# Performance work log

Measured on AMD Instinct MI355X. Metric: run time of the kernel, lower is better.

## Reference

```python
import jax
import jax.numpy as jnp
from jax import lax
import numpy as np

ALPHA_RISE = 0.5
ALPHA_FALL = 0.99


def setup_inputs() -> dict:
    key = jax.random.key(0)
    x = jax.random.normal(key, (16, 4096, 1024), dtype=jnp.float32)
    return {"x": x}


def reference(x):
    # x: [B, T, C]; asymmetric EMA scanned over T with data-dependent alpha.
    B, T, C = x.shape
    dt = x.dtype

    def step(carry, xt):
        y_prev, not_first = carry  # [B,C], [B,1]
        falling = (y_prev - xt > 0).astype(dt)  # Gt0: 1.0 if falling else 0.0
        alpha = falling * ALPHA_FALL + (1.0 - falling) * ALPHA_RISE
        y_upd = alpha * y_prev + (1.0 - alpha) * xt
        y = not_first * y_upd + (1.0 - not_first) * xt  # first frame passes x through
        return (y, jnp.ones_like(not_first)), y

    y0 = jnp.zeros((B, C), dt)
    nf0 = jnp.zeros((B, 1), dt)
    _, ys = lax.scan(step, (y0, nf0), jnp.swapaxes(x, 0, 1))  # ys: [T,B,C]
    return jnp.swapaxes(ys, 0, 1)
```

## Files before the change

### kernel.cpp

```cpp
#include <hip/hip_runtime.h>


constexpr int B = 16;
constexpr int T = 4096;
constexpr int C = 1024;
constexpr int U = 32;
constexpr int NSEQ = B * C;
constexpr int NCHUNK = 8;
constexpr int CHUNK = T / NCHUNK;
constexpr int WARM = 640;

__device__ inline float ema_step(float y, float xv) {
  const float d = y - xv;
  return fmaxf(__builtin_fmaf(0.99f, d, xv), __builtin_fmaf(0.5f, d, xv));
}

template <bool STORE>
__device__ inline void run_steps(const float* __restrict__ xp,
                                 float* __restrict__ op, float& y,
                                 int t_from, int t_to) {
  const int n = t_to - t_from;
  const int ngrp = n / U;
  const float* p = xp + (size_t)t_from * (size_t)C;
  float* q = op + (size_t)t_from * (size_t)C;

  float b0[U], b1[U];
  auto load = [&](float* buf, int g) {
    const float* pp = p + (size_t)g * (size_t)U * (size_t)C;
#pragma unroll
    for (int j = 0; j < U; ++j) buf[j] = pp[(size_t)j * (size_t)C];
  };
  auto comp = [&](const float* buf, int g) {
    float* qq = q + (size_t)g * (size_t)U * (size_t)C;
#pragma unroll
    for (int j = 0; j < U; ++j) {
      y = ema_step(y, buf[j]);
      if (STORE) qq[(size_t)j * (size_t)C] = y;
    }
  };

  if (ngrp >= 1) load(b0, 0);
  if (ngrp >= 2) load(b1, 1);
  int g = 0;
  while (g < ngrp) {
    comp(b0, g);
    if (g + 2 < ngrp) load(b0, g + 2);
    ++g;
    if (g >= ngrp) break;
    comp(b1, g);
    if (g + 2 < ngrp) load(b1, g + 2);
    ++g;
  }

  const int r = n - ngrp * U;
  if (r > 0) {
    float br[U];
    const float* pp = p + (size_t)ngrp * (size_t)U * (size_t)C;
    float* qq = q + (size_t)ngrp * (size_t)U * (size_t)C;
#pragma unroll
    for (int j = 0; j < U; ++j)
      if (j < r) br[j] = pp[(size_t)j * (size_t)C];
#pragma unroll
    for (int j = 0; j < U; ++j)
      if (j < r) {
        y = ema_step(y, br[j]);
        if (STORE) qq[(size_t)j * (size_t)C] = y;
      }
  }
}

__global__ __launch_bounds__(64) void AsymmetricEMA_kernel(
    const float* __restrict__ x, float* __restrict__ out) {
  const int tid = blockIdx.x * 64 + threadIdx.x;
  const int b = tid >> 10;
  const int c = tid & (C - 1);
  const size_t base = (size_t)b * (size_t)T * (size_t)C + (size_t)c;
  const float* __restrict__ xp = x + base;
  float* __restrict__ op = out + base;

  const int chunk = blockIdx.y;
  const int t_lo = chunk * CHUNK;
  const int t_hi = t_lo + CHUNK;

  if (chunk == 0) {
    float y = xp[0];
    op[0] = y;
    run_steps<true>(xp, op, y, 1, t_hi);
  } else {
    int s0 = t_lo - WARM;
    if (s0 < 0) s0 = 0;
    float y = xp[(size_t)s0 * (size_t)C];
    run_steps<false>(xp, op, y, s0 + 1, t_lo);
    run_steps<true>(xp, op, y, t_lo, t_hi);
  }
}

extern "C" void kernel_launch(void* const* d_in, const int* in_sizes, int n_in,
                              void* d_out, int out_size, void* d_ws, size_t ws_size,
                              hipStream_t stream) {
  const float* x = (const float*)d_in[0];
  float* out = (float*)d_out;
  dim3 grid(NSEQ / 64, NCHUNK);
  AsymmetricEMA_kernel<<<grid, 64, 0, stream>>>(x, out);
}
```

Baseline: 476.7 us.

## Vectorize EMA scan to float4 per thread and double time chunks

Each thread now handles four adjacent channels through float4 loads and stores, giving 128-bit memory transactions and fewer per-element address computations. To keep enough threads in flight with a quarter as many lanes, the time axis is split into 16 chunks instead of 8, and the unroll depth drops to 16 to limit register pressure. The extra chunks add more warm-up recomputation (WARM steps per chunk), which raises redundant read traffic. The warm-up also remains an approximation that depends on the EMA decay to converge.

```diff
diff --git a/kernel.cpp b/kernel.cpp
--- a/kernel.cpp
+++ b/kernel.cpp
@@ -4,38 +4,49 @@
 constexpr int B = 16;
 constexpr int T = 4096;
 constexpr int C = 1024;
-constexpr int U = 32;
-constexpr int NSEQ = B * C;
-constexpr int NCHUNK = 8;
+constexpr int VEC = 4;
+constexpr int CV = C / VEC;
+constexpr int U = 16;
+constexpr int NTHREADS = B * CV;
+constexpr int NCHUNK = 16;
 constexpr int CHUNK = T / NCHUNK;
 constexpr int WARM = 640;
 
-__device__ inline float ema_step(float y, float xv) {
+__device__ inline float ema1(float y, float xv) {
   const float d = y - xv;
   return fmaxf(__builtin_fmaf(0.99f, d, xv), __builtin_fmaf(0.5f, d, xv));
 }
 
+__device__ inline float4 ema4(float4 y, float4 xv) {
+  float4 r;
+  r.x = ema1(y.x, xv.x);
+  r.y = ema1(y.y, xv.y);
+  r.z = ema1(y.z, xv.z);
+  r.w = ema1(y.w, xv.w);
+  return r;
+}
+
 template <bool STORE>
-__device__ inline void run_steps(const float* __restrict__ xp,
-                                 float* __restrict__ op, float& y,
+__device__ inline void run_steps(const float4* __restrict__ xp,
+                                 float4* __restrict__ op, float4& y,
                                  int t_from, int t_to) {
   const int n = t_to - t_from;
   const int ngrp = n / U;
-  const float* p = xp + (size_t)t_from * (size_t)C;
-  float* q = op + (size_t)t_from * (size_t)C;
+  const float4* p = xp + (size_t)t_from * (size_t)CV;
+  float4* q = op + (size_t)t_from * (size_t)CV;
 
-  float b0[U], b1[U];
-  auto load = [&](float* buf, int g) {
-    const float* pp = p + (size_t)g * (size_t)U * (size_t)C;
+  float4 b0[U], b1[U];
+  auto load = [&](float4* buf, int g) {
+    const float4* pp = p + (size_t)g * (size_t)U * (size_t)CV;
 #pragma unroll
-    for (int j = 0; j < U; ++j) buf[j] = pp[(size_t)j * (size_t)C];
+    for (int j = 0; j < U; ++j) buf[j] = pp[(size_t)j * (size_t)CV];
   };
-  auto comp = [&](const float* buf, int g) {
-    float* qq = q + (size_t)g * (size_t)U * (size_t)C;
+  auto comp = [&](const float4* buf, int g) {
+    float4* qq = q + (size_t)g * (size_t)U * (size_t)CV;
 #pragma unroll
     for (int j = 0; j < U; ++j) {
-      y = ema_step(y, buf[j]);
-      if (STORE) qq[(size_t)j * (size_t)C] = y;
+      y = ema4(y, buf[j]);
+      if (STORE) qq[(size_t)j * (size_t)CV] = y;
     }
   };
 
@@ -54,42 +65,42 @@
 
   const int r = n - ngrp * U;
   if (r > 0) {
-    float br[U];
-    const float* pp = p + (size_t)ngrp * (size_t)U * (size_t)C;
-    float* qq = q + (size_t)ngrp * (size_t)U * (size_t)C;
+    float4 br[U];
+    const float4* pp = p + (size_t)ngrp * (size_t)U * (size_t)CV;
+    float4* qq = q + (size_t)ngrp * (size_t)U * (size_t)CV;
 #pragma unroll
     for (int j = 0; j < U; ++j)
-      if (j < r) br[j] = pp[(size_t)j * (size_t)C];
+      if (j < r) br[j] = pp[(size_t)j * (size_t)CV];
 #pragma unroll
     for (int j = 0; j < U; ++j)
       if (j < r) {
-        y = ema_step(y, br[j]);
-        if (STORE) qq[(size_t)j * (size_t)C] = y;
+        y = ema4(y, br[j]);
+        if (STORE) qq[(size_t)j * (size_t)CV] = y;
       }
   }
 }
 
 __global__ __launch_bounds__(64) void AsymmetricEMA_kernel(
-    const float* __restrict__ x, float* __restrict__ out) {
-  const int tid = blockIdx.x * 64 + threadIdx.x;
-  const int b = tid >> 10;
-  const int c = tid & (C - 1);
-  const size_t base = (size_t)b * (size_t)T * (size_t)C + (size_t)c;
-  const float* __restrict__ xp = x + base;
-  float* __restrict__ op = out + base;
+    const float4* __restrict__ x, float4* __restrict__ out) {
+  const int gid = blockIdx.x * 64 + threadIdx.x;
+  const int b = gid >> 8;
+  const int cv = gid & (CV - 1);
+  const size_t base = (size_t)b * (size_t)T * (size_t)CV + (size_t)cv;
+  const float4* __restrict__ xp = x + base;
+  float4* __restrict__ op = out + base;
 
   const int chunk = blockIdx.y;
   const int t_lo = chunk * CHUNK;
   const int t_hi = t_lo + CHUNK;
 
   if (chunk == 0) {
-    float y = xp[0];
+    float4 y = xp[0];
     op[0] = y;
     run_steps<true>(xp, op, y, 1, t_hi);
   } else {
     int s0 = t_lo - WARM;
     if (s0 < 0) s0 = 0;
-    float y = xp[(size_t)s0 * (size_t)C];
+    float4 y = xp[(size_t)s0 * (size_t)CV];
     run_steps<false>(xp, op, y, s0 + 1, t_lo);
     run_steps<true>(xp, op, y, t_lo, t_hi);
   }
@@ -98,8 +109,8 @@
 extern "C" void kernel_launch(void* const* d_in, const int* in_sizes, int n_in,
                               void* d_out, int out_size, void* d_ws, size_t ws_size,
                               hipStream_t stream) {
-  const float* x = (const float*)d_in[0];
-  float* out = (float*)d_out;
-  dim3 grid(NSEQ / 64, NCHUNK);
+  const float4* x = (const float4*)d_in[0];
+  float4* out = (float4*)d_out;
+  dim3 grid(NTHREADS / 64, NCHUNK);
   AsymmetricEMA_kernel<<<grid, 64, 0, stream>>>(x, out);
 }
```

Result: slower. 519.3 us (+8.9%).
